# Performance work log

Measured on AMD Instinct MI355X. Metric: run time of the kernel, lower is better.

The kernel has to match this reference:

```python
import jax, jax.numpy as jnp
import numpy as np

IN_DIM = 128
HID = 128
OUT = 128

def _linear(x, W, b):
    return x @ W + b

def setup_inputs() -> dict:
    key = jax.random.key(0)
    ks = jax.random.split(key, 16)
    B, N = 2, 512
    def w(k, fan_in, fan_out):
        lim = 1.0 / np.sqrt(fan_in)
        return jax.random.uniform(k, (fan_in, fan_out), jnp.float32, -lim, lim)
    def bvec(k, fan_in, fan_out):
        lim = 1.0 / np.sqrt(fan_in)
        return jax.random.uniform(k, (fan_out,), jnp.float32, -lim, lim)
    return {
        "features": jax.random.normal(ks[0], (B, N, IN_DIM), jnp.float32),
        "coords": jax.random.normal(ks[1], (B, N, 3), jnp.float32),
        "eW1": w(ks[2], 2 * IN_DIM + 1, HID), "eb1": bvec(ks[3], 2 * IN_DIM + 1, HID),
        "eW2": w(ks[4], HID, HID), "eb2": bvec(ks[5], HID, HID),
        "nW1": w(ks[6], IN_DIM + HID, HID), "nb1": bvec(ks[7], IN_DIM + HID, HID),
        "nW2": w(ks[8], HID, OUT), "nb2": bvec(ks[9], HID, OUT),
        "cW1": w(ks[10], HID, HID), "cb1": bvec(ks[11], HID, HID),
        "cW2": w(ks[12], HID, 1), "cb2": bvec(ks[13], HID, 1),
    }

def reference(features, coords, eW1, eb1, eW2, eb2, nW1, nb1, nW2, nb2, cW1, cb1, cW2, cb2):
    B, N, D = features.shape
    # pairwise coordinate differences and distances: (B, N, N, 3), (B, N, N, 1)
    coord_diff = coords[:, :, None, :] - coords[:, None, :, :]
    distances = jnp.sqrt(jnp.sum(coord_diff ** 2, axis=-1, keepdims=True) + 1e-8)
    # all-pairs edge features: (B, N, N, 2D+1)
    feat_i = jnp.broadcast_to(features[:, :, None, :], (B, N, N, D))
    feat_j = jnp.broadcast_to(features[:, None, :, :], (B, N, N, D))
    edge_features = jnp.concatenate([feat_i, feat_j, distances], axis=-1)
    edge_hidden = _linear(jax.nn.silu(_linear(edge_features, eW1, eb1)), eW2, eb2)
    # mean over neighbors j -> (B, N, HID)
    aggregated = jnp.mean(edge_hidden, axis=2)
    node_input = jnp.concatenate([features, aggregated], axis=-1)
    updated_features = _linear(jax.nn.silu(_linear(node_input, nW1, nb1)), nW2, nb2)
    # coordinate update
    coord_weights = _linear(jax.nn.silu(_linear(edge_hidden, cW1, cb1)), cW2, cb2)  # (B,N,N,1)
    updated_coords = coords + jnp.mean(coord_weights * coord_diff, axis=2)
    return (updated_features, updated_coords)
```

## Files before the change

### kernel.cpp

```cpp
#include <hip/hip_runtime.h>
#include <hip/hip_bf16.h>
#include <math.h>


typedef float f32x4 __attribute__((ext_vector_type(4)));
typedef short short8 __attribute__((ext_vector_type(8)));

#define MFMA16(a, b, c) __builtin_amdgcn_mfma_f32_16x16x32_bf16((a), (b), (c), 0, 0, 0)

__device__ __forceinline__ short f2bf(float x) {
    __hip_bfloat16 h = __float2bfloat16(x);
    union { __hip_bfloat16 h; short s; } v; v.h = h;
    return v.s;
}
__device__ __forceinline__ float bf2f(short s) {
    union { unsigned u; float f; } v; v.u = ((unsigned)(unsigned short)s) << 16;
    return v.f;
}
__device__ __forceinline__ float silu_f(float x) {
    return x * __builtin_amdgcn_rcpf(1.0f + __expf(-x));
}

__device__ __forceinline__ int swz(int row, int col) {
    int byte = (row << 8) | (col << 1);
    byte ^= (row & 7) << 4;
    return byte >> 1;
}

__global__ void egnn_prew(const float* __restrict__ feat, const float* __restrict__ eW1,
                          const float* __restrict__ eb1,
                          const float* __restrict__ eW2, const float* __restrict__ cW1,
                          const float* __restrict__ eb2, const float* __restrict__ cb1,
                          float* __restrict__ Abuf, float* __restrict__ Bbuf,
                          unsigned short* __restrict__ MbfT, float* __restrict__ bias2ws) {
    const int bid = blockIdx.x;
    const int t = threadIdx.x;
    if (bid < 1024) {
        __shared__ float f[128];
        if (t < 128) f[t] = feat[bid * 128 + t];
        __syncthreads();
        const int col  = t & 127;
        const int half = t >> 7;
        const float* W = eW1 + (size_t)half * 128 * 128 + col;
        float acc = half ? 0.f : eb1[col];
        #pragma unroll 8
        for (int k = 0; k < 128; ++k) acc += f[k] * W[(size_t)k * 128];
        if (half == 0) Abuf[bid * 128 + col] = acc;
        else           Bbuf[bid * 128 + col] = acc;
    } else {
        const int idx = (bid - 1024) * 2 + (t >> 7);
        const int c = t & 127;
        if (idx < 128) {
            float acc = 0.f;
            #pragma unroll 8
            for (int h = 0; h < 128; ++h) acc += eW2[idx * 128 + h] * cW1[h * 128 + c];
            MbfT[c * 128 + idx] = (unsigned short)f2bf(acc);
        } else if (idx == 128) {
            float acc = cb1[c];
            #pragma unroll 8
            for (int h = 0; h < 128; ++h) acc += eb2[h] * cW1[h * 128 + c];
            bias2ws[c] = acc;
        }
    }
}

__global__ void __launch_bounds__(256, 2) egnn_mainpost(
    const float* __restrict__ features, const float* __restrict__ coords,
    const float* __restrict__ eW1, const float* __restrict__ eW2,
    const float* __restrict__ eb2,
    const float* __restrict__ nW1, const float* __restrict__ nb1,
    const float* __restrict__ nW2, const float* __restrict__ nb2,
    const float* __restrict__ cW2, const float* __restrict__ cb2,
    const float* __restrict__ Abuf, const float* __restrict__ Bbuf,
    const unsigned short* __restrict__ MbfT, const float* __restrict__ bias2ws,
    float* __restrict__ out_feat, float* __restrict__ out_coord)
{
    constexpr int Nn = 512;
    __shared__ __align__(16) short se[64 * 128];
    __shared__ float aw[128], wd[128], pfi[128];
    __shared__ float cdp[2][3][64];
    __shared__ float warr[4][64];
    __shared__ float aggs[128], aggh[128], hbuf[128], part2[128];
    __shared__ float cred[4][3];
    __shared__ float ci3[3];

    float (*aggred)[128] = reinterpret_cast<float(*)[128]>(se);

    const int tid  = threadIdx.x;
    const int lane = tid & 63;
    const int wave = tid >> 6;
    const int node = blockIdx.x;
    const int b    = node >> 9;

    if (tid < 128) {
        aw[tid]  = Abuf[node * 128 + tid];
        wd[tid]  = eW1[256 * 128 + tid];
        pfi[tid] = features[node * 128 + tid];
    }
    if (tid == 0) {
        ci3[0] = coords[node * 3 + 0];
        ci3[1] = coords[node * 3 + 1];
        ci3[2] = coords[node * 3 + 2];
    }

    const int cfrag = wave * 32 + (lane & 15);
    const int koff  = (lane >> 4) * 8;
    short8 wfM[2][4];
    #pragma unroll
    for (int n2 = 0; n2 < 2; ++n2)
        #pragma unroll
        for (int k = 0; k < 4; ++k)
            wfM[n2][k] = *(const short8*)&MbfT[(size_t)(cfrag + n2 * 16) * 128 + k * 32 + koff];
    __syncthreads();

    const float b2_0  = bias2ws[cfrag], b2_1 = bias2ws[cfrag + 16];
    const float cw2_0 = cW2[cfrag],     cw2_1 = cW2[cfrag + 16];
    const float cb2v  = cb2[0];
    const float cix = ci3[0], ciy = ci3[1], ciz = ci3[2];

    const int jr = tid >> 2, cb = (tid & 3) * 32;
    const int rg = tid >> 4, c8 = (tid & 15) * 8;

    float ap[8];
    #pragma unroll
    for (int q = 0; q < 8; ++q) ap[q] = 0.f;
    float cax = 0.f, cay = 0.f, caz = 0.f;

    for (int t = 0; t < 8; ++t) {
        const int par = t & 1;
        {
            const int j = t * 64 + jr;
            const float dx = cix - coords[(b * Nn + j) * 3 + 0];
            const float dy = ciy - coords[(b * Nn + j) * 3 + 1];
            const float dz = ciz - coords[(b * Nn + j) * 3 + 2];
            const float dj = sqrtf(dx * dx + dy * dy + dz * dz + 1e-8f);
            if ((tid & 3) == 0) {
                cdp[par][0][jr] = dx; cdp[par][1][jr] = dy; cdp[par][2][jr] = dz;
            }
            const float* Bj = Bbuf + (size_t)(b * Nn + j) * 128 + cb;
            #pragma unroll
            for (int cc = 0; cc < 32; cc += 8) {
                f32x4 x0 = *(const f32x4*)(Bj + cc);
                f32x4 x1 = *(const f32x4*)(Bj + cc + 4);
                f32x4 a0 = *(const f32x4*)&aw[cb + cc];
                f32x4 a1 = *(const f32x4*)&aw[cb + cc + 4];
                f32x4 w0 = *(const f32x4*)&wd[cb + cc];
                f32x4 w1 = *(const f32x4*)&wd[cb + cc + 4];
                short8 v;
                #pragma unroll
                for (int r = 0; r < 4; ++r) v[r]     = f2bf(silu_f(a0[r] + x0[r] + dj * w0[r]));
                #pragma unroll
                for (int r = 0; r < 4; ++r) v[4 + r] = f2bf(silu_f(a1[r] + x1[r] + dj * w1[r]));
                *(short8*)&se[swz(jr, cb + cc)] = v;
            }
        }
        __syncthreads();

        f32x4 acc[4][2];
        #pragma unroll
        for (int m = 0; m < 4; ++m) {
            acc[m][0] = (f32x4){b2_0, b2_0, b2_0, b2_0};
            acc[m][1] = (f32x4){b2_1, b2_1, b2_1, b2_1};
        }
        #pragma unroll
        for (int m = 0; m < 4; ++m)
            #pragma unroll
            for (int k = 0; k < 4; ++k) {
                short8 a = *(const short8*)&se[swz(m * 16 + (lane & 15), k * 32 + koff)];
                acc[m][0] = MFMA16(a, wfM[0][k], acc[m][0]);
                acc[m][1] = MFMA16(a, wfM[1][k], acc[m][1]);
            }

        #pragma unroll
        for (int r = 0; r < 4; ++r) {
            short8 v = *(const short8*)&se[swz(rg * 4 + r, c8)];
            #pragma unroll
            for (int q = 0; q < 8; ++q) ap[q] += bf2f(v[q]);
        }

        #pragma unroll
        for (int m = 0; m < 4; ++m)
            #pragma unroll
            for (int reg = 0; reg < 4; ++reg) {
                float v = silu_f(acc[m][0][reg]) * cw2_0
                        + silu_f(acc[m][1][reg]) * cw2_1;
                union { float f; int i; } u, o;
                u.f = v; o.i = __builtin_amdgcn_mov_dpp(u.i, 0xB1, 0xF, 0xF, true); v += o.f;
                u.f = v; o.i = __builtin_amdgcn_mov_dpp(u.i, 0x4E, 0xF, 0xF, true); v += o.f;
                u.f = v; o.i = __builtin_amdgcn_ds_swizzle(u.i, 0x101F);            v += o.f;
                u.f = v; o.i = __builtin_amdgcn_ds_swizzle(u.i, 0x201F);            v += o.f;
                if ((lane & 15) == 0)
                    warr[wave][m * 16 + (lane >> 4) * 4 + reg] = v;
            }
        __syncthreads();

        if (lane < 16) {
            const int row = wave * 16 + lane;
            const float w = warr[0][row] + warr[1][row]
                          + warr[2][row] + warr[3][row] + cb2v;
            cax += w * cdp[par][0][row];
            cay += w * cdp[par][1][row];
            caz += w * cdp[par][2][row];
        }
    }

    #pragma unroll
    for (int q = 0; q < 8; ++q) aggred[rg][c8 + q] = ap[q];
    {
        float sx = cax, sy = cay, sz = caz;
        sx += __shfl_xor(sx, 1); sy += __shfl_xor(sy, 1); sz += __shfl_xor(sz, 1);
        sx += __shfl_xor(sx, 2); sy += __shfl_xor(sy, 2); sz += __shfl_xor(sz, 2);
        sx += __shfl_xor(sx, 4); sy += __shfl_xor(sy, 4); sz += __shfl_xor(sz, 4);
        sx += __shfl_xor(sx, 8); sy += __shfl_xor(sy, 8); sz += __shfl_xor(sz, 8);
        if (lane == 0) { cred[wave][0] = sx; cred[wave][1] = sy; cred[wave][2] = sz; }
    }
    __syncthreads();

    const int c = tid & 127, g = tid >> 7;
    if (tid < 128) {
        float s = 0.f;
        #pragma unroll
        for (int gg = 0; gg < 16; ++gg) s += aggred[gg][tid];
        aggs[tid] = s;
    }
    if (tid < 3) {
        out_coord[node * 3 + tid] = ci3[tid]
            + (cred[0][tid] + cred[1][tid] + cred[2][tid] + cred[3][tid]) * (1.f / 512.f);
    }
    __syncthreads();

    {
        float a2 = 0.f;
        #pragma unroll 8
        for (int k = g * 64; k < g * 64 + 64; ++k) a2 += aggs[k] * eW2[k * 128 + c];
        if (g == 1) part2[c] = a2;
        __syncthreads();
        if (g == 0) aggh[c] = (a2 + part2[c]) * (1.f / 512.f) + eb2[c];
        __syncthreads();
    }
    {
        float a2 = (g == 0) ? nb1[c] : 0.f;
        const float* src = (g == 0) ? pfi : aggh;
        const float* W = nW1 + (size_t)(g << 7) * 128 + c;
        #pragma unroll 8
        for (int k = 0; k < 128; ++k) a2 += src[k] * W[(size_t)k * 128];
        if (g == 1) part2[c] = a2;
        __syncthreads();
        if (g == 0) hbuf[c] = silu_f(a2 + part2[c]);
        __syncthreads();
    }
    {
        float a2 = (g == 0) ? nb2[c] : 0.f;
        #pragma unroll 8
        for (int k = g * 64; k < g * 64 + 64; ++k) a2 += hbuf[k] * nW2[k * 128 + c];
        if (g == 1) part2[c] = a2;
        __syncthreads();
        if (g == 0) out_feat[node * 128 + c] = a2 + part2[c];
    }
}

extern "C" void kernel_launch(void* const* d_in, const int* in_sizes, int n_in,
                              void* d_out, int out_size, void* d_ws, size_t ws_size,
                              hipStream_t stream)
{
    const float* features = (const float*)d_in[0];
    const float* coords   = (const float*)d_in[1];
    const float* eW1 = (const float*)d_in[2];
    const float* eb1 = (const float*)d_in[3];
    const float* eW2 = (const float*)d_in[4];
    const float* eb2 = (const float*)d_in[5];
    const float* nW1 = (const float*)d_in[6];
    const float* nb1 = (const float*)d_in[7];
    const float* nW2 = (const float*)d_in[8];
    const float* nb2 = (const float*)d_in[9];
    const float* cW1 = (const float*)d_in[10];
    const float* cb1 = (const float*)d_in[11];
    const float* cW2 = (const float*)d_in[12];
    const float* cb2 = (const float*)d_in[13];

    float* out = (float*)d_out;
    float* out_feat  = out;
    float* out_coord = out + 2 * 512 * 128;

    float* Abuf      = (float*)d_ws;
    float* Bbuf      = Abuf + 2 * 512 * 128;
    unsigned short* MbfT = (unsigned short*)(Bbuf + 2 * 512 * 128);
    float* bias2ws   = (float*)(MbfT + 128 * 128);

    egnn_prew<<<1089, 256, 0, stream>>>(features, eW1, eb1, eW2, cW1, eb2, cb1,
                                        Abuf, Bbuf, MbfT, bias2ws);
    egnn_mainpost<<<1024, 256, 0, stream>>>(features, coords, eW1, eW2, eb2,
                                            nW1, nb1, nW2, nb2, cW2, cb2,
                                            Abuf, Bbuf, MbfT, bias2ws,
                                            out_feat, out_coord);
}
```

Baseline: 178.2 us.

## Double-buffer edge tile and partial sums to drop a per-iteration barrier

The shared edge tile and the per-wave coordinate-weight partials are double-buffered, and the coordinate-diff buffer is triple-buffered. This lets the coordinate accumulation for tile t-1 run after the single barrier of tile t, so the second __syncthreads in each loop iteration goes away. The last tile's accumulation moves after the loop. The cost is doubling the edge-tile LDS footprint, which could limit occupancy, plus some extra modulo indexing.

```diff
diff --git a/kernel.cpp b/kernel.cpp
--- a/kernel.cpp
+++ b/kernel.cpp
@@ -76,15 +76,15 @@
     float* __restrict__ out_feat, float* __restrict__ out_coord)
 {
     constexpr int Nn = 512;
-    __shared__ __align__(16) short se[64 * 128];
+    __shared__ __align__(16) short se[2][64 * 128];
     __shared__ float aw[128], wd[128], pfi[128];
-    __shared__ float cdp[2][3][64];
-    __shared__ float warr[4][64];
+    __shared__ float cdp[3][3][64];
+    __shared__ float warr[2][4][64];
     __shared__ float aggs[128], aggh[128], hbuf[128], part2[128];
     __shared__ float cred[4][3];
     __shared__ float ci3[3];
 
-    float (*aggred)[128] = reinterpret_cast<float(*)[128]>(se);
+    float (*aggred)[128] = reinterpret_cast<float(*)[128]>(&se[0][0]);
 
     const int tid  = threadIdx.x;
     const int lane = tid & 63;
@@ -126,8 +126,10 @@
     for (int q = 0; q < 8; ++q) ap[q] = 0.f;
     float cax = 0.f, cay = 0.f, caz = 0.f;
 
+    #pragma unroll 2
     for (int t = 0; t < 8; ++t) {
-        const int par = t & 1;
+        const int p2 = t & 1;
+        const int p3 = t % 3;
         {
             const int j = t * 64 + jr;
             const float dx = cix - coords[(b * Nn + j) * 3 + 0];
@@ -135,7 +137,7 @@
             const float dz = ciz - coords[(b * Nn + j) * 3 + 2];
             const float dj = sqrtf(dx * dx + dy * dy + dz * dz + 1e-8f);
             if ((tid & 3) == 0) {
-                cdp[par][0][jr] = dx; cdp[par][1][jr] = dy; cdp[par][2][jr] = dz;
+                cdp[p3][0][jr] = dx; cdp[p3][1][jr] = dy; cdp[p3][2][jr] = dz;
             }
             const float* Bj = Bbuf + (size_t)(b * Nn + j) * 128 + cb;
             #pragma unroll
@@ -151,10 +153,20 @@
                 for (int r = 0; r < 4; ++r) v[r]     = f2bf(silu_f(a0[r] + x0[r] + dj * w0[r]));
                 #pragma unroll
                 for (int r = 0; r < 4; ++r) v[4 + r] = f2bf(silu_f(a1[r] + x1[r] + dj * w1[r]));
-                *(short8*)&se[swz(jr, cb + cc)] = v;
+                *(short8*)&se[p2][swz(jr, cb + cc)] = v;
             }
         }
         __syncthreads();
+
+        if (t > 0 && lane < 16) {
+            const int q2 = (t - 1) & 1, q3 = (t - 1) % 3;
+            const int row = wave * 16 + lane;
+            const float w = warr[q2][0][row] + warr[q2][1][row]
+                          + warr[q2][2][row] + warr[q2][3][row] + cb2v;
+            cax += w * cdp[q3][0][row];
+            cay += w * cdp[q3][1][row];
+            caz += w * cdp[q3][2][row];
+        }
 
         f32x4 acc[4][2];
         #pragma unroll
@@ -166,14 +178,14 @@
         for (int m = 0; m < 4; ++m)
             #pragma unroll
             for (int k = 0; k < 4; ++k) {
-                short8 a = *(const short8*)&se[swz(m * 16 + (lane & 15), k * 32 + koff)];
+                short8 a = *(const short8*)&se[p2][swz(m * 16 + (lane & 15), k * 32 + koff)];
                 acc[m][0] = MFMA16(a, wfM[0][k], acc[m][0]);
                 acc[m][1] = MFMA16(a, wfM[1][k], acc[m][1]);
             }
 
         #pragma unroll
         for (int r = 0; r < 4; ++r) {
-            short8 v = *(const short8*)&se[swz(rg * 4 + r, c8)];
+            short8 v = *(const short8*)&se[p2][swz(rg * 4 + r, c8)];
             #pragma unroll
             for (int q = 0; q < 8; ++q) ap[q] += bf2f(v[q]);
         }
@@ -190,18 +202,18 @@
                 u.f = v; o.i = __builtin_amdgcn_ds_swizzle(u.i, 0x101F);            v += o.f;
                 u.f = v; o.i = __builtin_amdgcn_ds_swizzle(u.i, 0x201F);            v += o.f;
                 if ((lane & 15) == 0)
-                    warr[wave][m * 16 + (lane >> 4) * 4 + reg] = v;
+                    warr[p2][wave][m * 16 + (lane >> 4) * 4 + reg] = v;
             }
-        __syncthreads();
-
-        if (lane < 16) {
-            const int row = wave * 16 + lane;
-            const float w = warr[0][row] + warr[1][row]
-                          + warr[2][row] + warr[3][row] + cb2v;
-            cax += w * cdp[par][0][row];
-            cay += w * cdp[par][1][row];
-            caz += w * cdp[par][2][row];
-        }
+    }
+    __syncthreads();
+
+    if (lane < 16) {
+        const int row = wave * 16 + lane;
+        const float w = warr[1][0][row] + warr[1][1][row]
+                      + warr[1][2][row] + warr[1][3][row] + cb2v;
+        cax += w * cdp[1][0][row];
+        cay += w * cdp[1][1][row];
+        caz += w * cdp[1][2][row];
     }
 
     #pragma unroll
```

New measurement: 182.3 us. 1.02x slower.
